# Optimization experiments

Measured on AMD Instinct MI355X. Metric: run time of the kernel, lower is better.

The kernel has to match this reference:

```python
import jax, jax.numpy as jnp
import numpy as np

B, T, C = 4, 2048, 768
H = 12  # n_head; head_dim = C // H = 64


def setup_inputs() -> dict:
    key = jax.random.key(0)
    k1, k2, k3, k4, k5 = jax.random.split(key, 5)
    scale = 0.02
    return {
        "x": jax.random.normal(k1, (B, T, C), dtype=jnp.float32),
        "w_attn": jax.random.normal(k2, (C, 3 * C), dtype=jnp.float32) * scale,
        "b_attn": jax.random.normal(k3, (3 * C,), dtype=jnp.float32) * scale,
        "w_proj": jax.random.normal(k4, (C, C), dtype=jnp.float32) * scale,
        "b_proj": jax.random.normal(k5, (C,), dtype=jnp.float32) * scale,
    }


def reference(x, w_attn, b_attn, w_proj, b_proj):
    Bx, Tx, Cx = x.shape
    hd = Cx // H  # head dim
    qkv = x @ w_attn + b_attn                       # [B, T, 3C]
    q, k, v = jnp.split(qkv, 3, axis=2)
    # [B, T, H, hd] -> [B, H, T, hd]
    q = q.reshape(Bx, Tx, H, hd).transpose(0, 2, 1, 3)
    k = k.reshape(Bx, Tx, H, hd).transpose(0, 2, 1, 3)
    v = v.reshape(Bx, Tx, H, hd).transpose(0, 2, 1, 3)
    att = jnp.einsum('bhqd,bhkd->bhqk', q, k) / jnp.sqrt(jnp.float32(hd))
    causal = jnp.tril(jnp.ones((Tx, Tx), dtype=bool))
    att = jnp.where(causal[None, None, :, :], att, -jnp.inf)
    att = jax.nn.softmax(att, axis=-1)
    y = jnp.einsum('bhqk,bhkd->bhqd', att, v)       # [B, H, T, hd]
    y = y.transpose(0, 2, 1, 3).reshape(Bx, Tx, Cx)
    return y @ w_proj + b_proj
```

## Files before the change

### kernel.cpp

```cpp
#include <hip/hip_runtime.h>
#include <hip/hip_bf16.h>

using f32x4 = __attribute__((ext_vector_type(4))) float;
using s16x8 = __attribute__((ext_vector_type(8))) short;

#define MFMA16x16x32(a, b, c) __builtin_amdgcn_mfma_f32_16x16x32_bf16((a), (b), (c), 0, 0, 0)

#define AS_G(p) ((const __attribute__((address_space(1))) void*)(p))
#define AS_L(p) ((__attribute__((address_space(3))) void*)(p))

#define BARRIER_LGKM() do { \
    asm volatile("s_waitcnt lgkmcnt(0)" ::: "memory"); \
    __builtin_amdgcn_s_barrier(); \
} while (0)

static __device__ __forceinline__ unsigned short f2bf(float f) {
    unsigned int u = __float_as_uint(f);
    u = (u + 0x7fffu + ((u >> 16) & 1u)) >> 16;
    return (unsigned short)u;
}
static __device__ __forceinline__ unsigned int cvt_pk_bf2(float lo, float hi) {
    unsigned int r;
    asm("v_cvt_pk_bf16_f32 %0, %1, %2" : "=v"(r) : "v"(lo), "v"(hi));
    return r;
}
static __device__ __forceinline__ int swz128(int r, int c) { return (r * 128 + c) ^ ((r & 7) << 4); }
static __device__ __forceinline__ int swz256v(int r, int c) { return (r * 256 + c) ^ ((r & 7) << 4); }

__global__ __launch_bounds__(256)
void prologue_kernel(const float* __restrict__ x, unsigned short* __restrict__ xb,
                     const float* __restrict__ w_attn, unsigned short* __restrict__ wTa,
                     const float* __restrict__ w_proj, unsigned short* __restrict__ wTp) {
    __shared__ float tile[32][33];
    const int bid = blockIdx.x, tid = threadIdx.x;
    if (bid < 2048) {
        const int n = 8192 * 768;
        int i = (bid * 256 + tid) * 4;
        const int stride = 2048 * 256 * 4;
        for (; i < n; i += stride) {
            float4 v = *(const float4*)(x + i);
            ushort4 o;
            o.x = f2bf(v.x); o.y = f2bf(v.y); o.z = f2bf(v.z); o.w = f2bf(v.w);
            *(ushort4*)(xb + i) = o;
        }
    } else {
        const float* w; unsigned short* wt; int K, N, bx, by;
        if (bid < 3776) {
            int id = bid - 2048; w = w_attn; wt = wTa; K = 768; N = 2304;
            bx = id % 72; by = id / 72;
        } else {
            int id = bid - 3776; w = w_proj; wt = wTp; K = 768; N = 768;
            bx = id % 24; by = id / 24;
        }
        const int tx = tid & 31, ty = tid >> 5;
        const int n0 = bx * 32, k0 = by * 32;
#pragma unroll
        for (int r = 0; r < 4; r++)
            tile[ty * 4 + r][tx] = w[(size_t)(k0 + ty * 4 + r) * N + n0 + tx];
        __syncthreads();
#pragma unroll
        for (int r = 0; r < 4; r++)
            wt[(size_t)(n0 + ty * 4 + r) * K + k0 + tx] = f2bf(tile[tx][ty * 4 + r]);
    }
}

template <bool OUT_BF16>
__global__ __launch_bounds__(256, 2)
void gemm_bt(const unsigned short* __restrict__ A, const unsigned short* __restrict__ Bt,
             const float* __restrict__ bias, void* __restrict__ Cout,
             unsigned short* __restrict__ Vt,
             int M, int N, int K, int ldc, int qcols, float qscale) {
    __shared__ char smem[65536];
    const int tid = threadIdx.x, wid = tid >> 6, lane = tid & 63;
    const int g = lane >> 4, lr = lane & 15;
    const int nx = N >> 7;
    const int ypx = (M >> 7) >> 3;
    const int xcd = blockIdx.x & 7, ii = blockIdx.x >> 3;
    const int m0 = (xcd * ypx + ii / nx) * 128;
    const int n0 = (ii % nx) * 128;
    const int wm = wid >> 1, wn = wid & 1;

    f32x4 acc[4][4];
#pragma unroll
    for (int i = 0; i < 4; i++)
#pragma unroll
        for (int j = 0; j < 4; j++) acc[i][j] = f32x4{0.f, 0.f, 0.f, 0.f};

    const int rbase = lane >> 3;
    const int cSw = ((lane & 7) << 4) ^ (rbase << 4);

    auto STAGE = [&](int buf, int kt) {
        char* base = smem + buf * 32768;
#pragma unroll
        for (int ww = 0; ww < 4; ww++) {
            int w = wid * 4 + ww;
            int r = w * 8 + rbase;
            const unsigned short* srcA = A + (size_t)(m0 + r) * K + kt + (cSw >> 1);
            __builtin_amdgcn_global_load_lds(AS_G(srcA), AS_L(base + w * 1024), 16, 0, 0);
            const unsigned short* srcB = Bt + (size_t)(n0 + r) * K + kt + (cSw >> 1);
            __builtin_amdgcn_global_load_lds(AS_G(srcB), AS_L(base + 16384 + w * 1024), 16, 0, 0);
        }
    };

    const int nk = K >> 6;
    STAGE(0, 0);

    for (int t = 0; t < nk; t++) {
        if (t + 1 < nk) {
            STAGE((t + 1) & 1, (t + 1) << 6);
            asm volatile("s_waitcnt vmcnt(8)" ::: "memory");
        } else {
            asm volatile("s_waitcnt vmcnt(0)" ::: "memory");
        }
        __builtin_amdgcn_s_barrier();
        char* cbase = smem + (t & 1) * 32768;
#pragma unroll
        for (int ks = 0; ks < 2; ks++) {
            s16x8 af[4], bfr[4];
#pragma unroll
            for (int i = 0; i < 4; i++)
                af[i] = *(const s16x8*)(cbase + swz128(wm * 64 + i * 16 + lr, ks * 64 + g * 16));
#pragma unroll
            for (int j = 0; j < 4; j++)
                bfr[j] = *(const s16x8*)(cbase + 16384 + swz128(wn * 64 + j * 16 + lr, ks * 64 + g * 16));
#pragma unroll
            for (int i = 0; i < 4; i++)
#pragma unroll
                for (int j = 0; j < 4; j++)
                    acc[i][j] = MFMA16x16x32(af[i], bfr[j], acc[i][j]);
        }
        BARRIER_LGKM();
    }

    if (Vt != nullptr && n0 >= 1536) {
#pragma unroll
        for (int j = 0; j < 4; j++) {
            int dl = wn * 64 + j * 16 + lr;
            float bv = bias[n0 + dl];
#pragma unroll
            for (int i = 0; i < 4; i++) {
                int tl = wm * 64 + i * 16 + g * 4;
                ushort4 o4;
                o4.x = f2bf(acc[i][j][0] + bv);
                o4.y = f2bf(acc[i][j][1] + bv);
                o4.z = f2bf(acc[i][j][2] + bv);
                o4.w = f2bf(acc[i][j][3] + bv);
                *(ushort4*)(smem + swz256v(dl, tl * 2)) = o4;
            }
        }
        __syncthreads();
        const int bb = m0 >> 11, t0 = m0 & 2047;
#pragma unroll
        for (int it = 0; it < 8; it++) {
            int dl = it * 16 + wid * 4 + g;
            int dg = (n0 - 1536) + dl;
            int hh = dg >> 6, dd = dg & 63;
            s16x8 v = *(const s16x8*)(smem + swz256v(dl, lr * 16));
            *(s16x8*)(Vt + ((((size_t)bb * 12 + hh) * 64 + dd) << 11) + t0 + lr * 8) = v;
        }
    } else {
#pragma unroll
        for (int j = 0; j < 4; j++) {
            int c = n0 + wn * 64 + j * 16 + lr;
            float bv = bias[c];
            float cscale = (c < qcols) ? qscale : 1.0f;
#pragma unroll
            for (int i = 0; i < 4; i++) {
#pragma unroll
                for (int rg = 0; rg < 4; rg++) {
                    int r = m0 + wm * 64 + i * 16 + g * 4 + rg;
                    float val = (acc[i][j][rg] + bv) * cscale;
                    if constexpr (OUT_BF16)
                        ((unsigned short*)Cout)[(size_t)r * ldc + c] = f2bf(val);
                    else
                        ((float*)Cout)[(size_t)r * ldc + c] = val;
                }
            }
        }
    }
}

__global__ __launch_bounds__(256, 2)
void attn_kernel(const unsigned short* __restrict__ qk, const unsigned short* __restrict__ Vt,
                 unsigned short* __restrict__ y) {
    __shared__ char smem[49152];
    const int tid = threadIdx.x, wid = tid >> 6, lane = tid & 63;
    const int g = lane >> 4, lr = lane & 15;
    const int T = 2048;

    const int s = blockIdx.x;
    const int xcd = s & 7, i = s >> 3;
    const int grp = xcd * 6 + (i >> 4);
    const int qpi = i & 15;
    const int h = grp % 12, b = grp / 12;
    const int qtA = qpi, qtB = 31 - qpi;
    const int q0A = qtA * 64, q0B = qtB * 64;

    const int krow = tid >> 2;
    const int kcol = (tid & 3) * 32;

    s16x8 vone;
#pragma unroll
    for (int e = 0; e < 8; e++) vone[e] = (short)0x3F80;

    const unsigned short* qrowA = qk + (size_t)(b * T + q0A + wid * 16 + lr) * 1536 + h * 64;
    const unsigned short* qrowB = qk + (size_t)(b * T + q0B + wid * 16 + lr) * 1536 + h * 64;
    s16x8 aqA[2], aqB[2];
    aqA[0] = *(const s16x8*)(qrowA + g * 8);
    aqA[1] = *(const s16x8*)(qrowA + 32 + g * 8);
    aqB[0] = *(const s16x8*)(qrowB + g * 8);
    aqB[1] = *(const s16x8*)(qrowB + 32 + g * 8);

    f32x4 oA[4], oB[4], lsumA, lsumB;
#pragma unroll
    for (int r = 0; r < 4; r++) { oA[r] = f32x4{0.f, 0.f, 0.f, 0.f}; oB[r] = f32x4{0.f, 0.f, 0.f, 0.f}; }
    lsumA = f32x4{0.f, 0.f, 0.f, 0.f};
    lsumB = f32x4{0.f, 0.f, 0.f, 0.f};

    const unsigned short* pkBase = qk + (size_t)(b * T + krow) * 1536 + 768 + h * 64 + (kcol >> 1);
    const unsigned short* pvBase = Vt + ((((size_t)b * 12 + h) * 64 + krow) << 11) + (kcol >> 1);

    const int ntA = qtA + 1, ntB = qtB + 1;

    s16x8 k0 = *(const s16x8*)(pkBase);
    s16x8 k1 = *(const s16x8*)(pkBase + 8);
    s16x8 v0 = *(const s16x8*)(pvBase);
    s16x8 v1 = *(const s16x8*)(pvBase + 8);
    *(s16x8*)(smem + swz128(krow, kcol)) = k0;
    *(s16x8*)(smem + swz128(krow, kcol + 16)) = k1;
    *(s16x8*)(smem + 16384 + swz128(krow, kcol)) = v0;
    *(s16x8*)(smem + 16384 + swz128(krow, kcol + 16)) = v1;
    if (ntB > 1) {
        const unsigned short* pk = pkBase + (size_t)64 * 1536;
        k0 = *(const s16x8*)(pk);
        k1 = *(const s16x8*)(pk + 8);
        const unsigned short* pv = pvBase + 64;
        v0 = *(const s16x8*)(pv);
        v1 = *(const s16x8*)(pv + 8);
    }
    BARRIER_LGKM();

    char* const pbaseB = smem + 32768 + wid * 2048;
    char* const pbaseA = smem + 40960 + wid * 2048;
    const int q_rel = wid * 16 + lr;

    for (int t = 0; t < ntB; t++) {
        char* kbase = smem + (t & 1) * 8192;
        char* vbase = smem + 16384 + (t & 1) * 8192;
        const bool actA = (t < ntA);

        {
            f32x4 st[4];
            __builtin_amdgcn_s_setprio(1);
#pragma unroll
            for (int nf = 0; nf < 4; nf++) {
                f32x4 sf = f32x4{0.f, 0.f, 0.f, 0.f};
#pragma unroll
                for (int ks = 0; ks < 2; ks++) {
                    s16x8 ak = *(const s16x8*)(kbase + swz128(nf * 16 + lr, (ks * 32 + g * 8) * 2));
                    sf = MFMA16x16x32(ak, aqB[ks], sf);
                }
                st[nf] = sf;
            }
            __builtin_amdgcn_s_setprio(0);
            const bool diag = (t == ntB - 1);
#pragma unroll
            for (int nf = 0; nf < 4; nf++)
#pragma unroll
                for (int rg = 0; rg < 4; rg++) {
                    float p = __builtin_amdgcn_exp2f(st[nf][rg]);
                    if (diag && (nf * 16 + g * 4 + rg > q_rel)) p = 0.f;
                    st[nf][rg] = p;
                }
#pragma unroll
            for (int nf = 0; nf < 4; nf++) {
                uint2 dw;
                dw.x = cvt_pk_bf2(st[nf][0], st[nf][1]);
                dw.y = cvt_pk_bf2(st[nf][2], st[nf][3]);
                *(uint2*)(pbaseB + swz128(lr, nf * 32 + g * 8)) = dw;
            }
        }
        if (actA) {
            f32x4 st[4];
            __builtin_amdgcn_s_setprio(1);
#pragma unroll
            for (int nf = 0; nf < 4; nf++) {
                f32x4 sf = f32x4{0.f, 0.f, 0.f, 0.f};
#pragma unroll
                for (int ks = 0; ks < 2; ks++) {
                    s16x8 ak = *(const s16x8*)(kbase + swz128(nf * 16 + lr, (ks * 32 + g * 8) * 2));
                    sf = MFMA16x16x32(ak, aqA[ks], sf);
                }
                st[nf] = sf;
            }
            __builtin_amdgcn_s_setprio(0);
            const bool diag = (t == ntA - 1);
#pragma unroll
            for (int nf = 0; nf < 4; nf++)
#pragma unroll
                for (int rg = 0; rg < 4; rg++) {
                    float p = __builtin_amdgcn_exp2f(st[nf][rg]);
                    if (diag && (nf * 16 + g * 4 + rg > q_rel)) p = 0.f;
                    st[nf][rg] = p;
                }
#pragma unroll
            for (int nf = 0; nf < 4; nf++) {
                uint2 dw;
                dw.x = cvt_pk_bf2(st[nf][0], st[nf][1]);
                dw.y = cvt_pk_bf2(st[nf][2], st[nf][3]);
                *(uint2*)(pbaseA + swz128(lr, nf * 32 + g * 8)) = dw;
            }
        }

        {
            s16x8 pf[2];
#pragma unroll
            for (int ks = 0; ks < 2; ks++)
                pf[ks] = *(const s16x8*)(pbaseB + swz128(lr, ks * 64 + g * 16));
            __builtin_amdgcn_s_setprio(1);
#pragma unroll
            for (int nf = 0; nf < 4; nf++) {
#pragma unroll
                for (int ks = 0; ks < 2; ks++) {
                    s16x8 bv = *(const s16x8*)(vbase + swz128(nf * 16 + lr, ks * 64 + g * 16));
                    oB[nf] = MFMA16x16x32(pf[ks], bv, oB[nf]);
                }
            }
            lsumB = MFMA16x16x32(pf[0], vone, lsumB);
            lsumB = MFMA16x16x32(pf[1], vone, lsumB);
            __builtin_amdgcn_s_setprio(0);
        }
        if (actA) {
            s16x8 pf[2];
#pragma unroll
            for (int ks = 0; ks < 2; ks++)
                pf[ks] = *(const s16x8*)(pbaseA + swz128(lr, ks * 64 + g * 16));
            __builtin_amdgcn_s_setprio(1);
#pragma unroll
            for (int nf = 0; nf < 4; nf++) {
#pragma unroll
                for (int ks = 0; ks < 2; ks++) {
                    s16x8 bv = *(const s16x8*)(vbase + swz128(nf * 16 + lr, ks * 64 + g * 16));
                    oA[nf] = MFMA16x16x32(pf[ks], bv, oA[nf]);
                }
            }
            lsumA = MFMA16x16x32(pf[0], vone, lsumA);
            lsumA = MFMA16x16x32(pf[1], vone, lsumA);
            __builtin_amdgcn_s_setprio(0);
        }

        if (t + 1 < ntB) {
            char* kn = smem + ((t + 1) & 1) * 8192;
            char* vn = smem + 16384 + ((t + 1) & 1) * 8192;
            *(s16x8*)(kn + swz128(krow, kcol)) = k0;
            *(s16x8*)(kn + swz128(krow, kcol + 16)) = k1;
            *(s16x8*)(vn + swz128(krow, kcol)) = v0;
            *(s16x8*)(vn + swz128(krow, kcol + 16)) = v1;
            if (t + 2 < ntB) {
                const unsigned short* pk = pkBase + (size_t)(t + 2) * 64 * 1536;
                k0 = *(const s16x8*)(pk);
                k1 = *(const s16x8*)(pk + 8);
                const unsigned short* pv = pvBase + (t + 2) * 64;
                v0 = *(const s16x8*)(pv);
                v1 = *(const s16x8*)(pv + 8);
            }
        }
        BARRIER_LGKM();
    }

#pragma unroll
    for (int which = 0; which < 2; which++) {
        const f32x4 lsum = which ? lsumB : lsumA;
        const int q0 = which ? q0B : q0A;
        f32x4* o = which ? oB : oA;
        float linv_q[4];
#pragma unroll
        for (int rg = 0; rg < 4; rg++) linv_q[rg] = 1.0f / lsum[rg];
#pragma unroll
        for (int nf = 0; nf < 4; nf++) {
#pragma unroll
            for (int rg = 0; rg < 4; rg++) {
                int row = b * T + q0 + wid * 16 + g * 4 + rg;
                int col = h * 64 + nf * 16 + lr;
                y[(size_t)row * 768 + col] = f2bf(o[nf][rg] * linv_q[rg]);
            }
        }
    }
}

extern "C" void kernel_launch(void* const* d_in, const int* in_sizes, int n_in,
                              void* d_out, int out_size, void* d_ws, size_t ws_size,
                              hipStream_t stream) {
    const float* x      = (const float*)d_in[0];
    const float* w_attn = (const float*)d_in[1];
    const float* b_attn = (const float*)d_in[2];
    const float* w_proj = (const float*)d_in[3];
    const float* b_proj = (const float*)d_in[4];

    char* ws = (char*)d_ws;
    unsigned short* qk  = (unsigned short*)(ws);
    unsigned short* Vt  = (unsigned short*)(ws + 25165824);
    unsigned short* wTa = (unsigned short*)(ws + 37748736);
    unsigned short* wTp = (unsigned short*)(ws + 41287680);

    const bool big = ws_size >= (size_t)55050240;
    unsigned short* xb = (unsigned short*)d_out;
    unsigned short* yb = big ? (unsigned short*)(ws + 42467328)
                             : (unsigned short*)((char*)d_out + 12582912);
    float* projOut = big ? (float*)d_out : (float*)ws;

    prologue_kernel<<<4352, 256, 0, stream>>>(x, xb, w_attn, wTa, w_proj, wTp);

    gemm_bt<true><<<1152, 256, 0, stream>>>(xb, wTa, b_attn, (void*)qk, Vt,
                                            8192, 2304, 768, 1536, 768, 0.1803368801111244f);
    attn_kernel<<<768, 256, 0, stream>>>(qk, Vt, yb);
    gemm_bt<false><<<384, 256, 0, stream>>>(yb, wTp, b_proj, (void*)projOut, nullptr,
                                            8192, 768, 768, 768, 0, 1.0f);
    if (!big)
        hipMemcpyAsync(d_out, projOut, 25165824, hipMemcpyDeviceToDevice, stream);
}
```

Before: 117.9 us.

## Fuse fp32-to-bf16 conversion of x into QKV GEMM A-tile loading

Removes the separate x conversion pass from the prologue kernel. The QKV GEMM now reads fp32 x directly into registers, converts it to bf16 with packed cvt instructions, and writes it to swizzled LDS, prefetching one k-tile ahead. This saves a full write and re-read of the bf16 copy of x. In exchange, the QKV GEMM reads twice the A bytes (and each A tile is re-read by 18 column blocks), uses more registers, and stages A through VGPRs instead of direct global-to-LDS loads.

```diff
diff --git a/kernel.cpp b/kernel.cpp
--- a/kernel.cpp
+++ b/kernel.cpp
@@ -28,45 +28,32 @@
 static __device__ __forceinline__ int swz256v(int r, int c) { return (r * 256 + c) ^ ((r & 7) << 4); }
 
 __global__ __launch_bounds__(256)
-void prologue_kernel(const float* __restrict__ x, unsigned short* __restrict__ xb,
-                     const float* __restrict__ w_attn, unsigned short* __restrict__ wTa,
+void prologue_kernel(const float* __restrict__ w_attn, unsigned short* __restrict__ wTa,
                      const float* __restrict__ w_proj, unsigned short* __restrict__ wTp) {
     __shared__ float tile[32][33];
     const int bid = blockIdx.x, tid = threadIdx.x;
-    if (bid < 2048) {
-        const int n = 8192 * 768;
-        int i = (bid * 256 + tid) * 4;
-        const int stride = 2048 * 256 * 4;
-        for (; i < n; i += stride) {
-            float4 v = *(const float4*)(x + i);
-            ushort4 o;
-            o.x = f2bf(v.x); o.y = f2bf(v.y); o.z = f2bf(v.z); o.w = f2bf(v.w);
-            *(ushort4*)(xb + i) = o;
-        }
+    const float* w; unsigned short* wt; int K, N, bx, by;
+    if (bid < 1728) {
+        w = w_attn; wt = wTa; K = 768; N = 2304;
+        bx = bid % 72; by = bid / 72;
     } else {
-        const float* w; unsigned short* wt; int K, N, bx, by;
-        if (bid < 3776) {
-            int id = bid - 2048; w = w_attn; wt = wTa; K = 768; N = 2304;
-            bx = id % 72; by = id / 72;
-        } else {
-            int id = bid - 3776; w = w_proj; wt = wTp; K = 768; N = 768;
-            bx = id % 24; by = id / 24;
-        }
-        const int tx = tid & 31, ty = tid >> 5;
-        const int n0 = bx * 32, k0 = by * 32;
-#pragma unroll
-        for (int r = 0; r < 4; r++)
-            tile[ty * 4 + r][tx] = w[(size_t)(k0 + ty * 4 + r) * N + n0 + tx];
-        __syncthreads();
-#pragma unroll
-        for (int r = 0; r < 4; r++)
-            wt[(size_t)(n0 + ty * 4 + r) * K + k0 + tx] = f2bf(tile[tx][ty * 4 + r]);
-    }
-}
-
-template <bool OUT_BF16>
+        int id = bid - 1728; w = w_proj; wt = wTp; K = 768; N = 768;
+        bx = id % 24; by = id / 24;
+    }
+    const int tx = tid & 31, ty = tid >> 5;
+    const int n0 = bx * 32, k0 = by * 32;
+#pragma unroll
+    for (int r = 0; r < 4; r++)
+        tile[ty * 4 + r][tx] = w[(size_t)(k0 + ty * 4 + r) * N + n0 + tx];
+    __syncthreads();
+#pragma unroll
+    for (int r = 0; r < 4; r++)
+        wt[(size_t)(n0 + ty * 4 + r) * K + k0 + tx] = f2bf(tile[tx][ty * 4 + r]);
+}
+
+template <bool OUT_BF16, bool AF32>
 __global__ __launch_bounds__(256, 2)
-void gemm_bt(const unsigned short* __restrict__ A, const unsigned short* __restrict__ Bt,
+void gemm_bt(const void* __restrict__ Ain, const unsigned short* __restrict__ Bt,
              const float* __restrict__ bias, void* __restrict__ Cout,
              unsigned short* __restrict__ Vt,
              int M, int N, int K, int ldc, int qcols, float qscale) {
@@ -89,47 +76,120 @@
     const int rbase = lane >> 3;
     const int cSw = ((lane & 7) << 4) ^ (rbase << 4);
 
-    auto STAGE = [&](int buf, int kt) {
-        char* base = smem + buf * 32768;
+    auto STAGE_B = [&](int buf, int kt) {
+        char* base = smem + buf * 32768 + 16384;
 #pragma unroll
         for (int ww = 0; ww < 4; ww++) {
             int w = wid * 4 + ww;
             int r = w * 8 + rbase;
-            const unsigned short* srcA = A + (size_t)(m0 + r) * K + kt + (cSw >> 1);
-            __builtin_amdgcn_global_load_lds(AS_G(srcA), AS_L(base + w * 1024), 16, 0, 0);
             const unsigned short* srcB = Bt + (size_t)(n0 + r) * K + kt + (cSw >> 1);
-            __builtin_amdgcn_global_load_lds(AS_G(srcB), AS_L(base + 16384 + w * 1024), 16, 0, 0);
+            __builtin_amdgcn_global_load_lds(AS_G(srcB), AS_L(base + w * 1024), 16, 0, 0);
         }
     };
 
     const int nk = K >> 6;
-    STAGE(0, 0);
-
-    for (int t = 0; t < nk; t++) {
-        if (t + 1 < nk) {
-            STAGE((t + 1) & 1, (t + 1) << 6);
-            asm volatile("s_waitcnt vmcnt(8)" ::: "memory");
-        } else {
-            asm volatile("s_waitcnt vmcnt(0)" ::: "memory");
-        }
-        __builtin_amdgcn_s_barrier();
-        char* cbase = smem + (t & 1) * 32768;
-#pragma unroll
-        for (int ks = 0; ks < 2; ks++) {
-            s16x8 af[4], bfr[4];
-#pragma unroll
-            for (int i = 0; i < 4; i++)
-                af[i] = *(const s16x8*)(cbase + swz128(wm * 64 + i * 16 + lr, ks * 64 + g * 16));
-#pragma unroll
-            for (int j = 0; j < 4; j++)
-                bfr[j] = *(const s16x8*)(cbase + 16384 + swz128(wn * 64 + j * 16 + lr, ks * 64 + g * 16));
-#pragma unroll
-            for (int i = 0; i < 4; i++)
+
+    if constexpr (AF32) {
+        const float* Af = (const float*)Ain;
+        const int ar = tid >> 1;
+        const int ach = tid & 1;
+        const float* aSrc = Af + (size_t)(m0 + ar) * K + ach * 32;
+
+        float4 areg[8];
+        auto LOAD_A = [&](int kt) {
+#pragma unroll
+            for (int i = 0; i < 8; i++)
+                areg[i] = *(const float4*)(aSrc + kt + i * 4);
+        };
+        auto WRITE_A = [&](int buf) {
+            char* base = smem + buf * 32768;
+#pragma unroll
+            for (int i = 0; i < 4; i++) {
+                uint4 dw;
+                dw.x = cvt_pk_bf2(areg[2 * i].x, areg[2 * i].y);
+                dw.y = cvt_pk_bf2(areg[2 * i].z, areg[2 * i].w);
+                dw.z = cvt_pk_bf2(areg[2 * i + 1].x, areg[2 * i + 1].y);
+                dw.w = cvt_pk_bf2(areg[2 * i + 1].z, areg[2 * i + 1].w);
+                *(uint4*)(base + swz128(ar, ach * 64 + i * 16)) = dw;
+            }
+        };
+
+        LOAD_A(0);
+        STAGE_B(0, 0);
+        WRITE_A(0);
+
+        for (int t = 0; t < nk; t++) {
+            if (t + 1 < nk) {
+                LOAD_A((t + 1) << 6);
+                STAGE_B((t + 1) & 1, (t + 1) << 6);
+                asm volatile("s_waitcnt vmcnt(12)" ::: "memory");
+            } else {
+                asm volatile("s_waitcnt vmcnt(0)" ::: "memory");
+            }
+            asm volatile("s_waitcnt lgkmcnt(0)" ::: "memory");
+            __builtin_amdgcn_s_barrier();
+            char* cbase = smem + (t & 1) * 32768;
+#pragma unroll
+            for (int ks = 0; ks < 2; ks++) {
+                s16x8 af[4], bfr[4];
+#pragma unroll
+                for (int i = 0; i < 4; i++)
+                    af[i] = *(const s16x8*)(cbase + swz128(wm * 64 + i * 16 + lr, ks * 64 + g * 16));
 #pragma unroll
                 for (int j = 0; j < 4; j++)
-                    acc[i][j] = MFMA16x16x32(af[i], bfr[j], acc[i][j]);
-        }
-        BARRIER_LGKM();
+                    bfr[j] = *(const s16x8*)(cbase + 16384 + swz128(wn * 64 + j * 16 + lr, ks * 64 + g * 16));
+#pragma unroll
+                for (int i = 0; i < 4; i++)
+#pragma unroll
+                    for (int j = 0; j < 4; j++)
+                        acc[i][j] = MFMA16x16x32(af[i], bfr[j], acc[i][j]);
+            }
+            if (t + 1 < nk) WRITE_A((t + 1) & 1);
+            BARRIER_LGKM();
+        }
+    } else {
+        const unsigned short* Ab = (const unsigned short*)Ain;
+        auto STAGE_A = [&](int buf, int kt) {
+            char* base = smem + buf * 32768;
+#pragma unroll
+            for (int ww = 0; ww < 4; ww++) {
+                int w = wid * 4 + ww;
+                int r = w * 8 + rbase;
+                const unsigned short* srcA = Ab + (size_t)(m0 + r) * K + kt + (cSw >> 1);
+                __builtin_amdgcn_global_load_lds(AS_G(srcA), AS_L(base + w * 1024), 16, 0, 0);
+            }
+        };
+
+        STAGE_A(0, 0);
+        STAGE_B(0, 0);
+
+        for (int t = 0; t < nk; t++) {
+            if (t + 1 < nk) {
+                STAGE_A((t + 1) & 1, (t + 1) << 6);
+                STAGE_B((t + 1) & 1, (t + 1) << 6);
+                asm volatile("s_waitcnt vmcnt(8)" ::: "memory");
+            } else {
+                asm volatile("s_waitcnt vmcnt(0)" ::: "memory");
+            }
+            __builtin_amdgcn_s_barrier();
+            char* cbase = smem + (t & 1) * 32768;
+#pragma unroll
+            for (int ks = 0; ks < 2; ks++) {
+                s16x8 af[4], bfr[4];
+#pragma unroll
+                for (int i = 0; i < 4; i++)
+                    af[i] = *(const s16x8*)(cbase + swz128(wm * 64 + i * 16 + lr, ks * 64 + g * 16));
+#pragma unroll
+                for (int j = 0; j < 4; j++)
+                    bfr[j] = *(const s16x8*)(cbase + 16384 + swz128(wn * 64 + j * 16 + lr, ks * 64 + g * 16));
+#pragma unroll
+                for (int i = 0; i < 4; i++)
+#pragma unroll
+                    for (int j = 0; j < 4; j++)
+                        acc[i][j] = MFMA16x16x32(af[i], bfr[j], acc[i][j]);
+            }
+            BARRIER_LGKM();
+        }
     }
 
     if (Vt != nullptr && n0 >= 1536) {
@@ -404,18 +464,17 @@
     unsigned short* wTp = (unsigned short*)(ws + 41287680);
 
     const bool big = ws_size >= (size_t)55050240;
-    unsigned short* xb = (unsigned short*)d_out;
     unsigned short* yb = big ? (unsigned short*)(ws + 42467328)
-                             : (unsigned short*)((char*)d_out + 12582912);
+                             : (unsigned short*)d_out;
     float* projOut = big ? (float*)d_out : (float*)ws;
 
-    prologue_kernel<<<4352, 256, 0, stream>>>(x, xb, w_attn, wTa, w_proj, wTp);
-
-    gemm_bt<true><<<1152, 256, 0, stream>>>(xb, wTa, b_attn, (void*)qk, Vt,
-                                            8192, 2304, 768, 1536, 768, 0.1803368801111244f);
+    prologue_kernel<<<2304, 256, 0, stream>>>(w_attn, wTa, w_proj, wTp);
+
+    gemm_bt<true, true><<<1152, 256, 0, stream>>>((const void*)x, wTa, b_attn, (void*)qk, Vt,
+                                                  8192, 2304, 768, 1536, 768, 0.1803368801111244f);
     attn_kernel<<<768, 256, 0, stream>>>(qk, Vt, yb);
-    gemm_bt<false><<<384, 256, 0, stream>>>(yb, wTp, b_proj, (void*)projOut, nullptr,
-                                            8192, 768, 768, 768, 0, 1.0f);
+    gemm_bt<false, false><<<384, 256, 0, stream>>>((const void*)yb, wTp, b_proj, (void*)projOut, nullptr,
+                                                   8192, 768, 768, 768, 0, 1.0f);
     if (!big)
         hipMemcpyAsync(d_out, projOut, 25165824, hipMemcpyDeviceToDevice, stream);
 }
```

After: 159.1 us. 1.35x slower.
